# Kernel tuning notes

Measured on AMD Instinct MI355X. Metric: run time of the kernel, lower is better.

## Reference

```python
import jax, jax.numpy as jnp
import numpy as np

IMAGE_SIZE = 256
MIN_DEPTH = 0.1
MAX_DEPTH = 10.0
WIN = 11  # SSIM window
C1 = 0.01 ** 2
C2 = 0.03 ** 2


def _avg_pool(x):
    # F.avg_pool2d(kernel=11, stride=1, pad=5, count_include_pad=True): zero-padded sum / 121
    s = jax.lax.reduce_window(x, 0.0, jax.lax.add,
                              (1, 1, WIN, WIN), (1, 1, 1, 1),
                              [(0, 0), (0, 0), (WIN // 2, WIN // 2), (WIN // 2, WIN // 2)])
    return s / (WIN * WIN)


def _project_points_to_depth(points, densities):
    # Vectorized weighted z-buffer scatter (replaces the per-point Python loop).
    B, N, _ = points.shape
    H = W = IMAGE_SIZE
    x, y, z = points[..., 0], points[..., 1], points[..., 2]
    w = jax.nn.sigmoid(densities[..., 0])                      # [B, N]
    z_safe = jnp.maximum(z, MIN_DEPTH)
    u_px = (x / z_safe + 0.5) * W                               # fx=fy=1, cx=cy=0.5
    v_px = (y / z_safe + 0.5) * H
    valid = (z > MIN_DEPTH) & (u_px >= 0) & (u_px < W) & (v_px >= 0) & (v_px < H)
    ui = jnp.clip(jnp.floor(u_px).astype(jnp.int32), 0, W - 1)
    vi = jnp.clip(jnp.floor(v_px).astype(jnp.int32), 0, H - 1)
    b_off = (jnp.arange(B, dtype=jnp.int32) * (H * W))[:, None]
    idx = (b_off + vi * W + ui).reshape(-1)                     # flat [B*N]
    wm = jnp.where(valid, w, 0.0).reshape(-1)
    zw = jnp.where(valid, z_safe * w, 0.0).reshape(-1)
    depth = jnp.zeros(B * H * W, points.dtype).at[idx].add(zw)
    wsum = jnp.zeros(B * H * W, points.dtype).at[idx].add(wm)
    depth = jnp.where(wsum > 0, depth / jnp.where(wsum > 0, wsum, 1.0), 0.0)
    return depth.reshape(B, 1, H, W)


def _normalize_depth(depth):
    # Per-batch min/max over valid (>0) pixels, clamped to [MIN_DEPTH, MAX_DEPTH].
    B = depth.shape[0]
    valid = depth > 0
    d = depth.reshape(B, -1)
    vm = valid.reshape(B, -1)
    has = vm.any(axis=1)
    vmin = jnp.min(jnp.where(vm, d, jnp.inf), axis=1)
    vmax = jnp.max(jnp.where(vm, d, -jnp.inf), axis=1)
    min_val = jnp.maximum(vmin, MIN_DEPTH)
    max_val = jnp.minimum(vmax, MAX_DEPTH)
    min_map = jnp.where(has, min_val, 0.0)[:, None, None, None]
    max_map = jnp.where(has, max_val, MAX_DEPTH)[:, None, None, None]
    return (depth - min_map) / (max_map - min_map + 1e-8) * valid.astype(depth.dtype)


def _ssim_loss(pred, target, mask):
    mu1 = _avg_pool(pred)
    mu2 = _avg_pool(target)
    mu1_sq, mu2_sq, mu1_mu2 = mu1 * mu1, mu2 * mu2, mu1 * mu2
    sigma1_sq = _avg_pool(pred * pred) - mu1_sq
    sigma2_sq = _avg_pool(target * target) - mu2_sq
    sigma12 = _avg_pool(pred * target) - mu1_mu2
    ssim_map = (2 * mu1_mu2 + C1) * (2 * sigma12 + C2) / ((mu1_sq + mu2_sq + C1) * (sigma1_sq + sigma2_sq + C2))
    ssim_map = ssim_map * mask
    return 1.0 - jnp.sum(ssim_map) / (jnp.sum(mask) + 1e-8)


def setup_inputs() -> dict:
    key = jax.random.key(0)
    k1, k2, k3 = jax.random.split(key, 3)
    B, N = 4, 2_000_000
    points = jax.random.normal(k1, (B, N, 3), dtype=jnp.float32)
    densities = jax.random.normal(k2, (B, N, 1), dtype=jnp.float32)
    depth_gt = jax.random.uniform(k3, (B, 1, IMAGE_SIZE, IMAGE_SIZE), dtype=jnp.float32)
    return {"points": points, "densities": densities, "depth_gt": depth_gt}


def reference(points, densities, depth_gt):
    depth_gt = jax.lax.stop_gradient(depth_gt)  # torch runs estimator under no_grad
    depth_gt = _normalize_depth(depth_gt)
    projected = _normalize_depth(_project_points_to_depth(points, densities))
    pred_mask = (projected > 0).astype(projected.dtype)
    gt_mask = (depth_gt > 0).astype(depth_gt.dtype)
    valid_mask = pred_mask * gt_mask
    msum = jnp.sum(valid_mask)
    l1 = jnp.sum(jnp.abs(projected * valid_mask - depth_gt * valid_mask)) / (msum + 1e-8)
    ssim = _ssim_loss(projected, depth_gt, valid_mask)
    total = jnp.minimum(0.8 * l1 + 0.2 * ssim, 1.0)
    return jnp.where(msum < 10, 0.0, total)
```

## Files before the change

### kernel.cpp

```cpp
#include <hip/hip_runtime.h>
#include <math.h>

#define HH 256
#define WW 256
static constexpr int HW = HH * WW;
static constexpr float MIN_D = 0.1f;
static constexpr float MAX_D = 10.0f;
static constexpr float C1c = 1e-4f;
static constexpr float C2c = 9e-4f;
static constexpr float ZW_SCALE = 1048576.f;
static constexpr float W_SCALE  = 4194304.f;

__device__ inline unsigned shdu(unsigned v, int o) {
    return (unsigned)__shfl_down((int)v, o, 64);
}

__global__ __launch_bounds__(256) void zero_k(ulonglong2* __restrict__ accv,
                          unsigned* __restrict__ mm, float* __restrict__ accum,
                          unsigned* __restrict__ ticket, int n16) {
    int i = blockIdx.x * 256 + threadIdx.x;
    if (i < n16) accv[i] = ulonglong2{0ull, 0ull};
    if (blockIdx.x == 0) {
        int tt = threadIdx.x;
        if (tt < 8) mm[tt] = 0xFFFFFFFFu;
        else if (tt < 16) mm[tt] = 0u;
        else if (tt < 19) accum[tt - 16] = 0.f;
        else if (tt == 19) *ticket = 0u;
    }
}

__global__ __launch_bounds__(256) void scatter_k(const float* __restrict__ pts,
                          const float* __restrict__ dens,
                          unsigned long long* __restrict__ acc,
                          int N4) {
    int t = blockIdx.x * 256 + threadIdx.x;
    if (t >= N4) return;
    int b = blockIdx.y;
    const float4* pb4 = (const float4*)(pts + (size_t)b * N4 * 12);
    const float4* db4 = (const float4*)(dens + (size_t)b * N4 * 4);
    unsigned long long* accb = acc + (size_t)b * HW;

    float4 A = pb4[3 * t], Bv = pb4[3 * t + 1], C = pb4[3 * t + 2];
    float4 D = db4[t];
    float xs[4] = {A.x, A.w, Bv.z, C.y};
    float ys[4] = {A.y, Bv.x, Bv.w, C.z};
    float zs[4] = {A.z, Bv.y, C.x, C.w};
    float ds[4] = {D.x, D.y, D.z, D.w};
#pragma unroll
    for (int j = 0; j < 4; ++j) {
        float z = zs[j];
        if (!(z > MIN_D)) continue;
        float invz = __builtin_amdgcn_rcpf(z);
        invz = invz * (2.0f - z * invz);
        float u = (xs[j] * invz + 0.5f) * (float)WW;
        float v = (ys[j] * invz + 0.5f) * (float)HH;
        if (!(u >= 0.f && u < (float)WW && v >= 0.f && v < (float)HH)) continue;
        int ui = (int)u;
        int vi = (int)v;
        float w = __builtin_amdgcn_rcpf(1.f + __expf(-ds[j]));
        unsigned hi = (unsigned)__float2int_rn(z * w * ZW_SCALE);
        unsigned lo = (unsigned)__float2int_rn(w * W_SCALE);
        unsigned long long pk = ((unsigned long long)hi << 32) | lo;
        atomicAdd(&accb[(vi << 8) | ui], pk);
    }
}

__global__ __launch_bounds__(256) void finalize_k(const unsigned long long* __restrict__ acc,
                           const float* __restrict__ gt, float* __restrict__ raw,
                           unsigned* __restrict__ mm) {
    int i = blockIdx.x * 256 + threadIdx.x;
    int b = blockIdx.x >> 8;
    unsigned long long v = acc[i];
    unsigned lo = (unsigned)v;
    unsigned hi = (unsigned)(v >> 32);
    float d = lo ? ((float)hi / (float)lo) * 4.0f : 0.f;
    raw[i] = d;
    float g = gt[i];
    unsigned dmin = d > 0.f ? __float_as_uint(d) : 0xFFFFFFFFu;
    unsigned dmax = d > 0.f ? __float_as_uint(d) : 0u;
    unsigned gmin = g > 0.f ? __float_as_uint(g) : 0xFFFFFFFFu;
    unsigned gmax = g > 0.f ? __float_as_uint(g) : 0u;
    for (int o = 32; o; o >>= 1) {
        dmin = min(dmin, shdu(dmin, o));
        gmin = min(gmin, shdu(gmin, o));
        dmax = max(dmax, shdu(dmax, o));
        gmax = max(gmax, shdu(gmax, o));
    }
    __shared__ unsigned sm[4][4];
    int wid = threadIdx.x >> 6, lane = threadIdx.x & 63;
    if (lane == 0) { sm[0][wid] = dmin; sm[1][wid] = gmin; sm[2][wid] = dmax; sm[3][wid] = gmax; }
    __syncthreads();
    if (threadIdx.x == 0) {
        unsigned m0 = min(min(sm[0][0], sm[0][1]), min(sm[0][2], sm[0][3]));
        unsigned m1 = min(min(sm[1][0], sm[1][1]), min(sm[1][2], sm[1][3]));
        unsigned m2 = max(max(sm[2][0], sm[2][1]), max(sm[2][2], sm[2][3]));
        unsigned m3 = max(max(sm[3][0], sm[3][1]), max(sm[3][2], sm[3][3]));
        atomicMin(&mm[b], m0);
        atomicMin(&mm[4 + b], m1);
        atomicMax(&mm[8 + b], m2);
        atomicMax(&mm[12 + b], m3);
    }
}

__global__ __launch_bounds__(256) void ssim_k(const float* __restrict__ raw,
                       const float* __restrict__ gt, const unsigned* __restrict__ mm,
                       float* __restrict__ accum, unsigned* __restrict__ ticket,
                       float* __restrict__ out, int nblocks) {
    __shared__ float hs[5][266];
    __shared__ float sb[3][4];
    int z = blockIdx.y;
    int r0 = blockIdx.x * 4;
    int tx = threadIdx.x;
    const float* P = raw + (size_t)z * HW;
    const float* T = gt + (size_t)z * HW;

    bool hasP = mm[8 + z] != 0u;
    float pmin_m = hasP ? fmaxf(__uint_as_float(mm[z]), MIN_D) : 0.f;
    float pscale = 1.f / ((hasP ? fminf(__uint_as_float(mm[8 + z]), MAX_D) : MAX_D) - pmin_m + 1e-8f);
    bool hasG = mm[12 + z] != 0u;
    float gmin_m = hasG ? fmaxf(__uint_as_float(mm[4 + z]), MIN_D) : 0.f;
    float gscale = 1.f / ((hasG ? fminf(__uint_as_float(mm[12 + z]), MAX_D) : MAX_D) - gmin_m + 1e-8f);

    float p[14], t[14];
#pragma unroll
    for (int i = 0; i < 14; ++i) {
        int row = r0 - 5 + i;
        bool ok = (row >= 0) && (row < HH);
        float dv = ok ? P[row * WW + tx] : 0.f;
        float gv = ok ? T[row * WW + tx] : 0.f;
        p[i] = (dv - pmin_m) * pscale * (dv > 0.f ? 1.f : 0.f);
        t[i] = (gv - gmin_m) * gscale * (gv > 0.f ? 1.f : 0.f);
    }
    if (tx < 5) {
#pragma unroll
        for (int q = 0; q < 5; ++q) { hs[q][tx] = 0.f; hs[q][261 + tx] = 0.f; }
    }
    __syncthreads();

    const float inv121 = 1.f / 121.f;
    float svA = 0.f, mA = 0.f, lvA = 0.f;
#pragma unroll
    for (int r = 0; r < 4; ++r) {
        float s1 = 0, s2 = 0, s11 = 0, s22 = 0, s12 = 0;
#pragma unroll
        for (int k = 0; k < 11; ++k) {
            float pp = p[r + k], tt = t[r + k];
            s1 += pp; s2 += tt;
            s11 = fmaf(pp, pp, s11); s22 = fmaf(tt, tt, s22); s12 = fmaf(pp, tt, s12);
        }
        hs[0][5 + tx] = s1; hs[1][5 + tx] = s2; hs[2][5 + tx] = s11;
        hs[3][5 + tx] = s22; hs[4][5 + tx] = s12;
        __syncthreads();
        float h1 = 0, h2 = 0, h11 = 0, h22 = 0, h12 = 0;
#pragma unroll
        for (int k = 0; k < 11; ++k) {
            h1 += hs[0][tx + k]; h2 += hs[1][tx + k]; h11 += hs[2][tx + k];
            h22 += hs[3][tx + k]; h12 += hs[4][tx + k];
        }
        float mu1 = h1 * inv121, mu2 = h2 * inv121;
        float mu1sq = mu1 * mu1, mu2sq = mu2 * mu2, mu12 = mu1 * mu2;
        float sig1 = h11 * inv121 - mu1sq;
        float sig2 = h22 * inv121 - mu2sq;
        float sig12 = h12 * inv121 - mu12;
        float smap = (2.f * mu12 + C1c) * (2.f * sig12 + C2c) /
                     ((mu1sq + mu2sq + C1c) * (sig1 + sig2 + C2c));
        float pc = p[r + 5], tc = t[r + 5];
        float m = (pc > 0.f && tc > 0.f) ? 1.f : 0.f;
        svA += smap * m;
        mA  += m;
        lvA += m * fabsf(pc - tc);
        __syncthreads();
    }

    for (int o = 32; o; o >>= 1) {
        svA += __shfl_down(svA, o, 64);
        mA  += __shfl_down(mA, o, 64);
        lvA += __shfl_down(lvA, o, 64);
    }
    int wid = tx >> 6, lane = tx & 63;
    if (lane == 0) { sb[0][wid] = svA; sb[1][wid] = mA; sb[2][wid] = lvA; }
    __syncthreads();
    if (tx == 0) {
        unsafeAtomicAdd(&accum[0], sb[0][0] + sb[0][1] + sb[0][2] + sb[0][3]);
        unsafeAtomicAdd(&accum[1], sb[1][0] + sb[1][1] + sb[1][2] + sb[1][3]);
        unsafeAtomicAdd(&accum[2], sb[2][0] + sb[2][1] + sb[2][2] + sb[2][3]);
        __threadfence();
        unsigned old = atomicAdd(ticket, 1u);
        if (old == (unsigned)(nblocks - 1)) {
            __threadfence();
            float ss = __hip_atomic_load(&accum[0], __ATOMIC_RELAXED, __HIP_MEMORY_SCOPE_AGENT);
            float ms = __hip_atomic_load(&accum[1], __ATOMIC_RELAXED, __HIP_MEMORY_SCOPE_AGENT);
            float ls = __hip_atomic_load(&accum[2], __ATOMIC_RELAXED, __HIP_MEMORY_SCOPE_AGENT);
            float l1   = ls / (ms + 1e-8f);
            float ssim = 1.f - ss / (ms + 1e-8f);
            float total = fminf(0.8f * l1 + 0.2f * ssim, 1.0f);
            out[0] = (ms < 10.f) ? 0.f : total;
        }
    }
}

extern "C" void kernel_launch(void* const* d_in, const int* in_sizes, int n_in,
                              void* d_out, int out_size, void* d_ws, size_t ws_size,
                              hipStream_t stream) {
    const float* pts = (const float*)d_in[0];
    const float* dens = (const float*)d_in[1];
    const float* gt = (const float*)d_in[2];
    int B = in_sizes[2] / HW;
    int N = in_sizes[1] / B;

    unsigned long long* acc = (unsigned long long*)d_ws;
    float* raw  = (float*)(acc + (size_t)B * HW);
    unsigned* mm = (unsigned*)(raw + (size_t)B * HW);
    float* accum = (float*)(mm + 16);
    unsigned* ticket = (unsigned*)(accum + 3);

    int n16 = B * HW / 2;
    zero_k<<<(n16 + 255) / 256, 256, 0, stream>>>((ulonglong2*)acc, mm, accum,
                                                  ticket, n16);

    int N4 = N / 4;
    scatter_k<<<dim3((N4 + 255) / 256, B), 256, 0, stream>>>(pts, dens, acc, N4);
    finalize_k<<<B * 256, 256, 0, stream>>>(acc, gt, raw, mm);
    int nblocks = 64 * B;
    ssim_k<<<dim3(64, B), 256, 0, stream>>>(raw, gt, mm, accum, ticket,
                                            (float*)d_out, nblocks);
}
```

Measured before the change: 106.6 us.

## Stage scatter inputs through LDS with global_load_lds and flatten batch grid

The scatter kernel now stages each block's 2048 points and densities into shared memory using direct global-to-LDS loads, then reads the fields from LDS with a per-thread stride. The grid is flattened across batches, and the batch index is computed per point from its global index. The aim is fully coalesced 16-byte loads with no stride-3 float4 gathers per thread. In exchange it adds 32KB of LDS per block, a barrier before any compute, and tail handling that zero-fills partial chunks. It also risks bank conflicts on the stride-3 LDS reads.

```diff
diff --git a/kernel.cpp b/kernel.cpp
--- a/kernel.cpp
+++ b/kernel.cpp
@@ -29,39 +29,67 @@
     }
 }
 
-__global__ __launch_bounds__(256) void scatter_k(const float* __restrict__ pts,
-                          const float* __restrict__ dens,
+__global__ __launch_bounds__(256) void scatter_k(const char* __restrict__ ptsB,
+                          const char* __restrict__ densB,
                           unsigned long long* __restrict__ acc,
-                          int N4) {
-    int t = blockIdx.x * 256 + threadIdx.x;
-    if (t >= N4) return;
-    int b = blockIdx.y;
-    const float4* pb4 = (const float4*)(pts + (size_t)b * N4 * 12);
-    const float4* db4 = (const float4*)(dens + (size_t)b * N4 * 4);
-    unsigned long long* accb = acc + (size_t)b * HW;
-
-    float4 A = pb4[3 * t], Bv = pb4[3 * t + 1], C = pb4[3 * t + 2];
-    float4 D = db4[t];
-    float xs[4] = {A.x, A.w, Bv.z, C.y};
-    float ys[4] = {A.y, Bv.x, Bv.w, C.z};
-    float zs[4] = {A.z, Bv.y, C.x, C.w};
-    float ds[4] = {D.x, D.y, D.z, D.w};
-#pragma unroll
-    for (int j = 0; j < 4; ++j) {
-        float z = zs[j];
+                          int N, int total) {
+    __shared__ float shp[6144];
+    __shared__ float shd[2048];
+    int tid = threadIdx.x;
+    int wave = tid >> 6, lane = tid & 63;
+    char* shpB = (char*)shp;
+    char* shdB = (char*)shd;
+    long long pbase = (long long)blockIdx.x * 24576;
+    long long dbase = (long long)blockIdx.x * 8192;
+    long long plim = (long long)total * 12;
+    long long dlim = (long long)total * 4;
+
+#pragma unroll
+    for (int i = 0; i < 6; ++i) {
+        int off = (wave * 6 + i) << 10;
+        long long g = pbase + off;
+        if (g + 1024 <= plim) {
+            __builtin_amdgcn_global_load_lds((const void*)(ptsB + g + (lane << 4)),
+                                             (void*)(shpB + off), 16, 0, 0);
+        } else {
+            *(float4*)(shpB + off + (lane << 4)) = float4{0.f, 0.f, 0.f, 0.f};
+        }
+    }
+#pragma unroll
+    for (int i = 0; i < 2; ++i) {
+        int off = (wave * 2 + i) << 10;
+        long long g = dbase + off;
+        if (g + 1024 <= dlim) {
+            __builtin_amdgcn_global_load_lds((const void*)(densB + g + (lane << 4)),
+                                             (void*)(shdB + off), 16, 0, 0);
+        } else {
+            *(float4*)(shdB + off + (lane << 4)) = float4{0.f, 0.f, 0.f, 0.f};
+        }
+    }
+    __syncthreads();
+
+    int p0 = blockIdx.x << 11;
+    int N2 = N << 1, N3 = N * 3;
+#pragma unroll
+    for (int k = 0; k < 8; ++k) {
+        int q = tid + (k << 8);
+        float z = shp[3 * q + 2];
         if (!(z > MIN_D)) continue;
+        float x = shp[3 * q], y = shp[3 * q + 1];
         float invz = __builtin_amdgcn_rcpf(z);
         invz = invz * (2.0f - z * invz);
-        float u = (xs[j] * invz + 0.5f) * (float)WW;
-        float v = (ys[j] * invz + 0.5f) * (float)HH;
+        float u = (x * invz + 0.5f) * (float)WW;
+        float v = (y * invz + 0.5f) * (float)HH;
         if (!(u >= 0.f && u < (float)WW && v >= 0.f && v < (float)HH)) continue;
         int ui = (int)u;
         int vi = (int)v;
-        float w = __builtin_amdgcn_rcpf(1.f + __expf(-ds[j]));
+        float w = __builtin_amdgcn_rcpf(1.f + __expf(-shd[q]));
         unsigned hi = (unsigned)__float2int_rn(z * w * ZW_SCALE);
         unsigned lo = (unsigned)__float2int_rn(w * W_SCALE);
         unsigned long long pk = ((unsigned long long)hi << 32) | lo;
-        atomicAdd(&accb[(vi << 8) | ui], pk);
+        int p = p0 + q;
+        int b = (p >= N) + (p >= N2) + (p >= N3);
+        atomicAdd(&acc[b * HW + ((vi << 8) | ui)], pk);
     }
 }
 
@@ -207,6 +235,7 @@
     const float* gt = (const float*)d_in[2];
     int B = in_sizes[2] / HW;
     int N = in_sizes[1] / B;
+    int total = B * N;
 
     unsigned long long* acc = (unsigned long long*)d_ws;
     float* raw  = (float*)(acc + (size_t)B * HW);
@@ -218,8 +247,9 @@
     zero_k<<<(n16 + 255) / 256, 256, 0, stream>>>((ulonglong2*)acc, mm, accum,
                                                   ticket, n16);
 
-    int N4 = N / 4;
-    scatter_k<<<dim3((N4 + 255) / 256, B), 256, 0, stream>>>(pts, dens, acc, N4);
+    int nsblk = (total + 2047) / 2048;
+    scatter_k<<<nsblk, 256, 0, stream>>>((const char*)pts, (const char*)dens,
+                                         acc, N, total);
     finalize_k<<<B * 256, 256, 0, stream>>>(acc, gt, raw, mm);
     int nblocks = 64 * B;
     ssim_k<<<dim3(64, B), 256, 0, stream>>>(raw, gt, mm, accum, ticket,
```

Result: slower. 110.1 us (+3.3%).

## Fuse all stages into one persistent kernel with software grid barriers

Applied to the files above, without the earlier changes.

Replaces the zero, scatter, finalize and SSIM kernels with a single persistent kernel that runs each stage as grid-stride work separated by atomic grid barriers. A tiny init kernel resets the barrier state. This aims to remove inter-kernel launch gaps and tail effects. In exchange it adds barrier spin costs, relies on all blocks being co-resident, and hardcodes four batches in the min/max reduction.

```diff
diff --git a/kernel.cpp b/kernel.cpp
--- a/kernel.cpp
+++ b/kernel.cpp
@@ -14,188 +14,235 @@
 __device__ inline unsigned shdu(unsigned v, int o) {
     return (unsigned)__shfl_down((int)v, o, 64);
 }
-
-__global__ __launch_bounds__(256) void zero_k(ulonglong2* __restrict__ accv,
-                          unsigned* __restrict__ mm, float* __restrict__ accum,
-                          unsigned* __restrict__ ticket, int n16) {
-    int i = blockIdx.x * 256 + threadIdx.x;
-    if (i < n16) accv[i] = ulonglong2{0ull, 0ull};
-    if (blockIdx.x == 0) {
-        int tt = threadIdx.x;
-        if (tt < 8) mm[tt] = 0xFFFFFFFFu;
-        else if (tt < 16) mm[tt] = 0u;
-        else if (tt < 19) accum[tt - 16] = 0.f;
-        else if (tt == 19) *ticket = 0u;
-    }
-}
-
-__global__ __launch_bounds__(256) void scatter_k(const float* __restrict__ pts,
-                          const float* __restrict__ dens,
-                          unsigned long long* __restrict__ acc,
-                          int N4) {
-    int t = blockIdx.x * 256 + threadIdx.x;
-    if (t >= N4) return;
-    int b = blockIdx.y;
-    const float4* pb4 = (const float4*)(pts + (size_t)b * N4 * 12);
-    const float4* db4 = (const float4*)(dens + (size_t)b * N4 * 4);
-    unsigned long long* accb = acc + (size_t)b * HW;
-
-    float4 A = pb4[3 * t], Bv = pb4[3 * t + 1], C = pb4[3 * t + 2];
-    float4 D = db4[t];
-    float xs[4] = {A.x, A.w, Bv.z, C.y};
-    float ys[4] = {A.y, Bv.x, Bv.w, C.z};
-    float zs[4] = {A.z, Bv.y, C.x, C.w};
-    float ds[4] = {D.x, D.y, D.z, D.w};
-#pragma unroll
-    for (int j = 0; j < 4; ++j) {
-        float z = zs[j];
-        if (!(z > MIN_D)) continue;
-        float invz = __builtin_amdgcn_rcpf(z);
-        invz = invz * (2.0f - z * invz);
-        float u = (xs[j] * invz + 0.5f) * (float)WW;
-        float v = (ys[j] * invz + 0.5f) * (float)HH;
-        if (!(u >= 0.f && u < (float)WW && v >= 0.f && v < (float)HH)) continue;
-        int ui = (int)u;
-        int vi = (int)v;
-        float w = __builtin_amdgcn_rcpf(1.f + __expf(-ds[j]));
-        unsigned hi = (unsigned)__float2int_rn(z * w * ZW_SCALE);
-        unsigned lo = (unsigned)__float2int_rn(w * W_SCALE);
-        unsigned long long pk = ((unsigned long long)hi << 32) | lo;
-        atomicAdd(&accb[(vi << 8) | ui], pk);
-    }
-}
-
-__global__ __launch_bounds__(256) void finalize_k(const unsigned long long* __restrict__ acc,
-                           const float* __restrict__ gt, float* __restrict__ raw,
-                           unsigned* __restrict__ mm) {
-    int i = blockIdx.x * 256 + threadIdx.x;
-    int b = blockIdx.x >> 8;
-    unsigned long long v = acc[i];
-    unsigned lo = (unsigned)v;
-    unsigned hi = (unsigned)(v >> 32);
-    float d = lo ? ((float)hi / (float)lo) * 4.0f : 0.f;
-    raw[i] = d;
-    float g = gt[i];
-    unsigned dmin = d > 0.f ? __float_as_uint(d) : 0xFFFFFFFFu;
-    unsigned dmax = d > 0.f ? __float_as_uint(d) : 0u;
-    unsigned gmin = g > 0.f ? __float_as_uint(g) : 0xFFFFFFFFu;
-    unsigned gmax = g > 0.f ? __float_as_uint(g) : 0u;
-    for (int o = 32; o; o >>= 1) {
-        dmin = min(dmin, shdu(dmin, o));
-        gmin = min(gmin, shdu(gmin, o));
-        dmax = max(dmax, shdu(dmax, o));
-        gmax = max(gmax, shdu(gmax, o));
-    }
-    __shared__ unsigned sm[4][4];
-    int wid = threadIdx.x >> 6, lane = threadIdx.x & 63;
-    if (lane == 0) { sm[0][wid] = dmin; sm[1][wid] = gmin; sm[2][wid] = dmax; sm[3][wid] = gmax; }
+__device__ inline float shdf(float v, int o) {
+    return __shfl_down(v, o, 64);
+}
+
+__device__ inline void grid_barrier(unsigned* __restrict__ bar, int nblk) {
     __syncthreads();
     if (threadIdx.x == 0) {
-        unsigned m0 = min(min(sm[0][0], sm[0][1]), min(sm[0][2], sm[0][3]));
-        unsigned m1 = min(min(sm[1][0], sm[1][1]), min(sm[1][2], sm[1][3]));
-        unsigned m2 = max(max(sm[2][0], sm[2][1]), max(sm[2][2], sm[2][3]));
-        unsigned m3 = max(max(sm[3][0], sm[3][1]), max(sm[3][2], sm[3][3]));
-        atomicMin(&mm[b], m0);
-        atomicMin(&mm[4 + b], m1);
-        atomicMax(&mm[8 + b], m2);
-        atomicMax(&mm[12 + b], m3);
-    }
-}
-
-__global__ __launch_bounds__(256) void ssim_k(const float* __restrict__ raw,
-                       const float* __restrict__ gt, const unsigned* __restrict__ mm,
-                       float* __restrict__ accum, unsigned* __restrict__ ticket,
-                       float* __restrict__ out, int nblocks) {
+        __threadfence();
+        unsigned g = __hip_atomic_load(&bar[1], __ATOMIC_RELAXED, __HIP_MEMORY_SCOPE_AGENT);
+        unsigned old = __hip_atomic_fetch_add(&bar[0], 1u, __ATOMIC_ACQ_REL, __HIP_MEMORY_SCOPE_AGENT);
+        if (old == (unsigned)(nblk - 1)) {
+            __hip_atomic_store(&bar[0], 0u, __ATOMIC_RELAXED, __HIP_MEMORY_SCOPE_AGENT);
+            __hip_atomic_store(&bar[1], g + 1u, __ATOMIC_RELEASE, __HIP_MEMORY_SCOPE_AGENT);
+        } else {
+            while (__hip_atomic_load(&bar[1], __ATOMIC_ACQUIRE, __HIP_MEMORY_SCOPE_AGENT) == g)
+                __builtin_amdgcn_s_sleep(2);
+        }
+    }
+    __syncthreads();
+}
+
+__global__ void init_k(unsigned* __restrict__ bar) {
+    if (threadIdx.x < 2) bar[threadIdx.x] = 0u;
+}
+
+__global__ __launch_bounds__(256) void mono_k(
+        const float* __restrict__ pts, const float* __restrict__ dens,
+        const float* __restrict__ gt, unsigned long long* __restrict__ acc,
+        float* __restrict__ raw, unsigned* __restrict__ mm,
+        float* __restrict__ accum, unsigned* __restrict__ ticket,
+        unsigned* __restrict__ bar, float* __restrict__ out,
+        int N, int total, int nblk) {
     __shared__ float hs[5][266];
     __shared__ float sb[3][4];
-    int z = blockIdx.y;
-    int r0 = blockIdx.x * 4;
-    int tx = threadIdx.x;
-    const float* P = raw + (size_t)z * HW;
-    const float* T = gt + (size_t)z * HW;
-
-    bool hasP = mm[8 + z] != 0u;
-    float pmin_m = hasP ? fmaxf(__uint_as_float(mm[z]), MIN_D) : 0.f;
-    float pscale = 1.f / ((hasP ? fminf(__uint_as_float(mm[8 + z]), MAX_D) : MAX_D) - pmin_m + 1e-8f);
-    bool hasG = mm[12 + z] != 0u;
-    float gmin_m = hasG ? fmaxf(__uint_as_float(mm[4 + z]), MIN_D) : 0.f;
-    float gscale = 1.f / ((hasG ? fminf(__uint_as_float(mm[12 + z]), MAX_D) : MAX_D) - gmin_m + 1e-8f);
-
-    float p[14], t[14];
-#pragma unroll
-    for (int i = 0; i < 14; ++i) {
-        int row = r0 - 5 + i;
-        bool ok = (row >= 0) && (row < HH);
-        float dv = ok ? P[row * WW + tx] : 0.f;
-        float gv = ok ? T[row * WW + tx] : 0.f;
-        p[i] = (dv - pmin_m) * pscale * (dv > 0.f ? 1.f : 0.f);
-        t[i] = (gv - gmin_m) * gscale * (gv > 0.f ? 1.f : 0.f);
-    }
-    if (tx < 5) {
-#pragma unroll
-        for (int q = 0; q < 5; ++q) { hs[q][tx] = 0.f; hs[q][261 + tx] = 0.f; }
-    }
-    __syncthreads();
-
-    const float inv121 = 1.f / 121.f;
-    float svA = 0.f, mA = 0.f, lvA = 0.f;
-#pragma unroll
-    for (int r = 0; r < 4; ++r) {
-        float s1 = 0, s2 = 0, s11 = 0, s22 = 0, s12 = 0;
-#pragma unroll
-        for (int k = 0; k < 11; ++k) {
-            float pp = p[r + k], tt = t[r + k];
-            s1 += pp; s2 += tt;
-            s11 = fmaf(pp, pp, s11); s22 = fmaf(tt, tt, s22); s12 = fmaf(pp, tt, s12);
-        }
-        hs[0][5 + tx] = s1; hs[1][5 + tx] = s2; hs[2][5 + tx] = s11;
-        hs[3][5 + tx] = s22; hs[4][5 + tx] = s12;
+    __shared__ unsigned sm[4][4];
+
+    const int tid  = threadIdx.x;
+    const int gtid = blockIdx.x * 256 + tid;
+    const int GSZ  = gridDim.x * 256;
+    const int B    = total / N;
+    const int BHW  = B * HW;
+
+    for (int i = gtid; i < BHW; i += GSZ)
+        __hip_atomic_store(&acc[i], 0ull, __ATOMIC_RELAXED, __HIP_MEMORY_SCOPE_AGENT);
+    if (gtid < 8)        __hip_atomic_store(&mm[gtid], 0xFFFFFFFFu, __ATOMIC_RELAXED, __HIP_MEMORY_SCOPE_AGENT);
+    else if (gtid < 16)  __hip_atomic_store(&mm[gtid], 0u, __ATOMIC_RELAXED, __HIP_MEMORY_SCOPE_AGENT);
+    else if (gtid < 19)  __hip_atomic_store(&accum[gtid - 16], 0.f, __ATOMIC_RELAXED, __HIP_MEMORY_SCOPE_AGENT);
+    else if (gtid == 19) __hip_atomic_store(ticket, 0u, __ATOMIC_RELAXED, __HIP_MEMORY_SCOPE_AGENT);
+    grid_barrier(bar, nblk);
+
+    {
+        const float4* p4 = (const float4*)pts;
+        const float4* d4 = (const float4*)dens;
+        int total4 = total >> 2;
+        int N2 = N << 1, N3 = N * 3;
+        for (int g = gtid; g < total4; g += GSZ) {
+            float4 A = p4[3 * g], Bv = p4[3 * g + 1], C = p4[3 * g + 2];
+            float4 D = d4[g];
+            float xs[4] = {A.x, A.w, Bv.z, C.y};
+            float ys[4] = {A.y, Bv.x, Bv.w, C.z};
+            float zs[4] = {A.z, Bv.y, C.x, C.w};
+            float ds[4] = {D.x, D.y, D.z, D.w};
+            int p0 = g << 2;
+            int b = (p0 >= N) + (p0 >= N2) + (p0 >= N3);
+            unsigned long long* accb = acc + (size_t)b * HW;
+#pragma unroll
+            for (int j = 0; j < 4; ++j) {
+                float z = zs[j];
+                if (!(z > MIN_D)) continue;
+                float invz = __builtin_amdgcn_rcpf(z);
+                invz = invz * (2.0f - z * invz);
+                float u = (xs[j] * invz + 0.5f) * (float)WW;
+                float v = (ys[j] * invz + 0.5f) * (float)HH;
+                if (!(u >= 0.f && u < (float)WW && v >= 0.f && v < (float)HH)) continue;
+                int ui = (int)u;
+                int vi = (int)v;
+                float w = __builtin_amdgcn_rcpf(1.f + __expf(-ds[j]));
+                unsigned hi = (unsigned)__float2int_rn(z * w * ZW_SCALE);
+                unsigned lo = (unsigned)__float2int_rn(w * W_SCALE);
+                atomicAdd(&accb[(vi << 8) | ui],
+                          ((unsigned long long)hi << 32) | lo);
+            }
+        }
+    }
+    grid_barrier(bar, nblk);
+
+    {
+        unsigned dmin[4] = {0xFFFFFFFFu, 0xFFFFFFFFu, 0xFFFFFFFFu, 0xFFFFFFFFu};
+        unsigned dmax[4] = {0, 0, 0, 0};
+        unsigned gmn[4]  = {0xFFFFFFFFu, 0xFFFFFFFFu, 0xFFFFFFFFu, 0xFFFFFFFFu};
+        unsigned gmx[4]  = {0, 0, 0, 0};
+        for (int i = gtid; i < BHW; i += GSZ) {
+            int b = i >> 16;
+            unsigned long long v = __hip_atomic_load(&acc[i], __ATOMIC_RELAXED,
+                                                     __HIP_MEMORY_SCOPE_AGENT);
+            unsigned lo = (unsigned)v;
+            unsigned hi = (unsigned)(v >> 32);
+            float d = lo ? ((float)hi / (float)lo) * 4.0f : 0.f;
+            __hip_atomic_store(&raw[i], d, __ATOMIC_RELAXED, __HIP_MEMORY_SCOPE_AGENT);
+            float g = gt[i];
+            if (d > 0.f) {
+                unsigned du = __float_as_uint(d);
+                dmin[b] = min(dmin[b], du); dmax[b] = max(dmax[b], du);
+            }
+            if (g > 0.f) {
+                unsigned gu = __float_as_uint(g);
+                gmn[b] = min(gmn[b], gu); gmx[b] = max(gmx[b], gu);
+            }
+        }
+#pragma unroll
+        for (int b = 0; b < 4; ++b) {
+            unsigned a0 = dmin[b], a1 = gmn[b], a2 = dmax[b], a3 = gmx[b];
+            for (int o = 32; o; o >>= 1) {
+                a0 = min(a0, shdu(a0, o)); a1 = min(a1, shdu(a1, o));
+                a2 = max(a2, shdu(a2, o)); a3 = max(a3, shdu(a3, o));
+            }
+            int wid = tid >> 6, lane = tid & 63;
+            if (lane == 0) { sm[0][wid] = a0; sm[1][wid] = a1; sm[2][wid] = a2; sm[3][wid] = a3; }
+            __syncthreads();
+            if (tid == 0) {
+                unsigned m0 = min(min(sm[0][0], sm[0][1]), min(sm[0][2], sm[0][3]));
+                unsigned m1 = min(min(sm[1][0], sm[1][1]), min(sm[1][2], sm[1][3]));
+                unsigned m2 = max(max(sm[2][0], sm[2][1]), max(sm[2][2], sm[2][3]));
+                unsigned m3 = max(max(sm[3][0], sm[3][1]), max(sm[3][2], sm[3][3]));
+                if (m0 != 0xFFFFFFFFu) atomicMin(&mm[b], m0);
+                if (m1 != 0xFFFFFFFFu) atomicMin(&mm[4 + b], m1);
+                if (m2) atomicMax(&mm[8 + b], m2);
+                if (m3) atomicMax(&mm[12 + b], m3);
+            }
+            __syncthreads();
+        }
+    }
+    grid_barrier(bar, nblk);
+
+    const int nb = B * 64;
+    for (int band = blockIdx.x; band < nb; band += gridDim.x) {
+        int z  = band >> 6;
+        int r0 = (band & 63) * 4;
+        int tx = tid;
+        const float* P = raw + (size_t)z * HW;
+        const float* T = gt + (size_t)z * HW;
+
+        unsigned mmz0 = __hip_atomic_load(&mm[z],      __ATOMIC_RELAXED, __HIP_MEMORY_SCOPE_AGENT);
+        unsigned mmz1 = __hip_atomic_load(&mm[4 + z],  __ATOMIC_RELAXED, __HIP_MEMORY_SCOPE_AGENT);
+        unsigned mmz2 = __hip_atomic_load(&mm[8 + z],  __ATOMIC_RELAXED, __HIP_MEMORY_SCOPE_AGENT);
+        unsigned mmz3 = __hip_atomic_load(&mm[12 + z], __ATOMIC_RELAXED, __HIP_MEMORY_SCOPE_AGENT);
+        bool hasP = mmz2 != 0u;
+        float pmin_m = hasP ? fmaxf(__uint_as_float(mmz0), MIN_D) : 0.f;
+        float pscale = 1.f / ((hasP ? fminf(__uint_as_float(mmz2), MAX_D) : MAX_D) - pmin_m + 1e-8f);
+        bool hasG = mmz3 != 0u;
+        float gmin_m = hasG ? fmaxf(__uint_as_float(mmz1), MIN_D) : 0.f;
+        float gscale = 1.f / ((hasG ? fminf(__uint_as_float(mmz3), MAX_D) : MAX_D) - gmin_m + 1e-8f);
+
+        float p[14], t[14];
+#pragma unroll
+        for (int i = 0; i < 14; ++i) {
+            int row = r0 - 5 + i;
+            bool ok = (row >= 0) && (row < HH);
+            float dv = ok ? __hip_atomic_load(&P[row * WW + tx], __ATOMIC_RELAXED,
+                                              __HIP_MEMORY_SCOPE_AGENT) : 0.f;
+            float gv = ok ? T[row * WW + tx] : 0.f;
+            p[i] = (dv - pmin_m) * pscale * (dv > 0.f ? 1.f : 0.f);
+            t[i] = (gv - gmin_m) * gscale * (gv > 0.f ? 1.f : 0.f);
+        }
+        if (tx < 5) {
+#pragma unroll
+            for (int q = 0; q < 5; ++q) { hs[q][tx] = 0.f; hs[q][261 + tx] = 0.f; }
+        }
         __syncthreads();
-        float h1 = 0, h2 = 0, h11 = 0, h22 = 0, h12 = 0;
-#pragma unroll
-        for (int k = 0; k < 11; ++k) {
-            h1 += hs[0][tx + k]; h2 += hs[1][tx + k]; h11 += hs[2][tx + k];
-            h22 += hs[3][tx + k]; h12 += hs[4][tx + k];
-        }
-        float mu1 = h1 * inv121, mu2 = h2 * inv121;
-        float mu1sq = mu1 * mu1, mu2sq = mu2 * mu2, mu12 = mu1 * mu2;
-        float sig1 = h11 * inv121 - mu1sq;
-        float sig2 = h22 * inv121 - mu2sq;
-        float sig12 = h12 * inv121 - mu12;
-        float smap = (2.f * mu12 + C1c) * (2.f * sig12 + C2c) /
-                     ((mu1sq + mu2sq + C1c) * (sig1 + sig2 + C2c));
-        float pc = p[r + 5], tc = t[r + 5];
-        float m = (pc > 0.f && tc > 0.f) ? 1.f : 0.f;
-        svA += smap * m;
-        mA  += m;
-        lvA += m * fabsf(pc - tc);
+
+        const float inv121 = 1.f / 121.f;
+        float svA = 0.f, mA = 0.f, lvA = 0.f;
+#pragma unroll
+        for (int r = 0; r < 4; ++r) {
+            float s1 = 0, s2 = 0, s11 = 0, s22 = 0, s12 = 0;
+#pragma unroll
+            for (int k = 0; k < 11; ++k) {
+                float pp = p[r + k], tt = t[r + k];
+                s1 += pp; s2 += tt;
+                s11 = fmaf(pp, pp, s11); s22 = fmaf(tt, tt, s22); s12 = fmaf(pp, tt, s12);
+            }
+            hs[0][5 + tx] = s1; hs[1][5 + tx] = s2; hs[2][5 + tx] = s11;
+            hs[3][5 + tx] = s22; hs[4][5 + tx] = s12;
+            __syncthreads();
+            float h1 = 0, h2 = 0, h11 = 0, h22 = 0, h12 = 0;
+#pragma unroll
+            for (int k = 0; k < 11; ++k) {
+                h1 += hs[0][tx + k]; h2 += hs[1][tx + k]; h11 += hs[2][tx + k];
+                h22 += hs[3][tx + k]; h12 += hs[4][tx + k];
+            }
+            float mu1 = h1 * inv121, mu2 = h2 * inv121;
+            float mu1sq = mu1 * mu1, mu2sq = mu2 * mu2, mu12 = mu1 * mu2;
+            float sig1 = h11 * inv121 - mu1sq;
+            float sig2 = h22 * inv121 - mu2sq;
+            float sig12 = h12 * inv121 - mu12;
+            float smap = (2.f * mu12 + C1c) * (2.f * sig12 + C2c) /
+                         ((mu1sq + mu2sq + C1c) * (sig1 + sig2 + C2c));
+            float pc = p[r + 5], tc = t[r + 5];
+            float m = (pc > 0.f && tc > 0.f) ? 1.f : 0.f;
+            svA += smap * m;
+            mA  += m;
+            lvA += m * fabsf(pc - tc);
+            __syncthreads();
+        }
+
+        for (int o = 32; o; o >>= 1) {
+            svA += shdf(svA, o); mA += shdf(mA, o); lvA += shdf(lvA, o);
+        }
+        int wid = tx >> 6, lane = tx & 63;
+        if (lane == 0) { sb[0][wid] = svA; sb[1][wid] = mA; sb[2][wid] = lvA; }
         __syncthreads();
-    }
-
-    for (int o = 32; o; o >>= 1) {
-        svA += __shfl_down(svA, o, 64);
-        mA  += __shfl_down(mA, o, 64);
-        lvA += __shfl_down(lvA, o, 64);
-    }
-    int wid = tx >> 6, lane = tx & 63;
-    if (lane == 0) { sb[0][wid] = svA; sb[1][wid] = mA; sb[2][wid] = lvA; }
-    __syncthreads();
-    if (tx == 0) {
-        unsafeAtomicAdd(&accum[0], sb[0][0] + sb[0][1] + sb[0][2] + sb[0][3]);
-        unsafeAtomicAdd(&accum[1], sb[1][0] + sb[1][1] + sb[1][2] + sb[1][3]);
-        unsafeAtomicAdd(&accum[2], sb[2][0] + sb[2][1] + sb[2][2] + sb[2][3]);
-        __threadfence();
-        unsigned old = atomicAdd(ticket, 1u);
-        if (old == (unsigned)(nblocks - 1)) {
+        if (tx == 0) {
+            unsafeAtomicAdd(&accum[0], sb[0][0] + sb[0][1] + sb[0][2] + sb[0][3]);
+            unsafeAtomicAdd(&accum[1], sb[1][0] + sb[1][1] + sb[1][2] + sb[1][3]);
+            unsafeAtomicAdd(&accum[2], sb[2][0] + sb[2][1] + sb[2][2] + sb[2][3]);
             __threadfence();
-            float ss = __hip_atomic_load(&accum[0], __ATOMIC_RELAXED, __HIP_MEMORY_SCOPE_AGENT);
-            float ms = __hip_atomic_load(&accum[1], __ATOMIC_RELAXED, __HIP_MEMORY_SCOPE_AGENT);
-            float ls = __hip_atomic_load(&accum[2], __ATOMIC_RELAXED, __HIP_MEMORY_SCOPE_AGENT);
-            float l1   = ls / (ms + 1e-8f);
-            float ssim = 1.f - ss / (ms + 1e-8f);
-            float total = fminf(0.8f * l1 + 0.2f * ssim, 1.0f);
-            out[0] = (ms < 10.f) ? 0.f : total;
-        }
+            unsigned old = atomicAdd(ticket, 1u);
+            if (old == (unsigned)(nb - 1)) {
+                __threadfence();
+                float ss = __hip_atomic_load(&accum[0], __ATOMIC_RELAXED, __HIP_MEMORY_SCOPE_AGENT);
+                float ms = __hip_atomic_load(&accum[1], __ATOMIC_RELAXED, __HIP_MEMORY_SCOPE_AGENT);
+                float ls = __hip_atomic_load(&accum[2], __ATOMIC_RELAXED, __HIP_MEMORY_SCOPE_AGENT);
+                float l1   = ls / (ms + 1e-8f);
+                float ssim = 1.f - ss / (ms + 1e-8f);
+                float total_l = fminf(0.8f * l1 + 0.2f * ssim, 1.0f);
+                out[0] = (ms < 10.f) ? 0.f : total_l;
+            }
+        }
+        __syncthreads();
     }
 }
 
@@ -207,21 +254,27 @@
     const float* gt = (const float*)d_in[2];
     int B = in_sizes[2] / HW;
     int N = in_sizes[1] / B;
+    int total = B * N;
+    int BHW = B * HW;
 
     unsigned long long* acc = (unsigned long long*)d_ws;
-    float* raw  = (float*)(acc + (size_t)B * HW);
-    unsigned* mm = (unsigned*)(raw + (size_t)B * HW);
+    float* raw  = (float*)(acc + (size_t)BHW);
+    unsigned* mm = (unsigned*)(raw + (size_t)BHW);
     float* accum = (float*)(mm + 16);
     unsigned* ticket = (unsigned*)(accum + 3);
-
-    int n16 = B * HW / 2;
-    zero_k<<<(n16 + 255) / 256, 256, 0, stream>>>((ulonglong2*)acc, mm, accum,
-                                                  ticket, n16);
-
-    int N4 = N / 4;
-    scatter_k<<<dim3((N4 + 255) / 256, B), 256, 0, stream>>>(pts, dens, acc, N4);
-    finalize_k<<<B * 256, 256, 0, stream>>>(acc, gt, raw, mm);
-    int nblocks = 64 * B;
-    ssim_k<<<dim3(64, B), 256, 0, stream>>>(raw, gt, mm, accum, ticket,
-                                            (float*)d_out, nblocks);
-}
+    unsigned* bar = (unsigned*)(((char*)(ticket + 1)) + 108);
+    float* outp = (float*)d_out;
+
+    int maxb = 0;
+    (void)hipOccupancyMaxActiveBlocksPerMultiprocessor(&maxb, (const void*)mono_k, 256, 0);
+    int ncu = 0;
+    (void)hipDeviceGetAttribute(&ncu, hipDeviceAttributeMultiprocessorCount, 0);
+    if (maxb < 1) maxb = 1;
+    if (ncu < 1) ncu = 256;
+    long long grid_ll = (long long)maxb * ncu;
+    int grid = (int)(grid_ll < 256 ? 256 : (grid_ll > 1024 ? 1024 : grid_ll));
+
+    init_k<<<1, 64, 0, stream>>>(bar);
+    mono_k<<<grid, 256, 0, stream>>>(pts, dens, gt, acc, raw, mm, accum, ticket,
+                                     bar, outp, N, total, grid);
+}
```

Result: slower. 265.2 us (+148.8%).
